# Optimization experiments

Hardware: AMD Instinct MI355X
Metric: run time of the kernel (lower is better)

The kernel has to match this reference:

```python
import jax, jax.numpy as jnp
import numpy as np

HEADS = 8
DIM_HEAD = 64
SCALE = DIM_HEAD ** -0.5

def _split_heads(x):
    # [B, N, H*D] -> [B, H, N, D]
    B, N, _ = x.shape
    return x.reshape(B, N, HEADS, DIM_HEAD).transpose(0, 2, 1, 3)

def _merge_heads(x):
    # [B, H, N, D] -> [B, N, H*D]
    B, H, N, D = x.shape
    return x.transpose(0, 2, 1, 3).reshape(B, N, H * D)

def setup_inputs() -> dict:
    key = jax.random.key(0)
    ks = jax.random.split(key, 6)
    B, N, DIM = 4, 2048, 512
    INNER = HEADS * DIM_HEAD
    return {
        "query1": jax.random.normal(ks[0], (B, N, DIM), dtype=jnp.float32),
        "query2": jax.random.normal(ks[1], (B, N, DIM), dtype=jnp.float32),
        "key_value": jax.random.normal(ks[2], (B, N, DIM), dtype=jnp.float32),
        "Wq1": jax.random.normal(ks[3], (DIM, INNER), dtype=jnp.float32) * (DIM ** -0.5),
        "Wq2": jax.random.normal(ks[4], (DIM, INNER), dtype=jnp.float32) * (DIM ** -0.5),
        "Wkv": jax.random.normal(ks[5], (DIM, 2 * INNER), dtype=jnp.float32) * (DIM ** -0.5),
    }

def reference(query1, query2, key_value, Wq1, Wq2, Wkv):
    q1 = _split_heads(query1 @ Wq1)          # [B,H,N,D]
    q2 = _split_heads(query2 @ Wq2)          # [B,H,N,D]
    kv = key_value @ Wkv                     # [B,N,2*inner]
    k_, v_ = jnp.split(kv, 2, axis=-1)
    k = _split_heads(k_)                     # [B,H,N,D]
    v = _split_heads(v_)                     # [B,H,N,D]
    dots1 = jnp.einsum('bhnd,bhmd->bhnm', q1, k) * SCALE
    dots2 = jnp.einsum('bhnd,bhmd->bhnm', q2, k) * SCALE
    attn1 = jax.nn.softmax(dots1, axis=-1)
    attn2 = jax.nn.softmax(dots2, axis=-1)
    out1 = _merge_heads(jnp.einsum('bhnm,bhmd->bhnd', attn1, v))
    out2 = _merge_heads(jnp.einsum('bhnm,bhmd->bhnd', attn2, v))
    return (out1, out2)
```

## Files before the change

kernel.cpp:

```cpp
#include <hip/hip_runtime.h>
#include <hip/hip_bf16.h>
#include <stdint.h>

typedef __attribute__((ext_vector_type(8))) short bf16x8;
typedef __attribute__((ext_vector_type(4))) float f32x4;
typedef __attribute__((ext_vector_type(4))) int int4v;
typedef __attribute__((ext_vector_type(2))) unsigned int uint2v;

#define MFMA16(a,b,c) __builtin_amdgcn_mfma_f32_16x16x32_bf16((a),(b),(c),0,0,0)

__device__ __forceinline__ unsigned short f2bf(float x) {
  unsigned u = __float_as_uint(x);
  u += 0x7FFFu + ((u >> 16) & 1u);
  return (unsigned short)(u >> 16);
}

__global__ __launch_bounds__(256) void convWT_kernel(
    const float* __restrict__ Wq1, const float* __restrict__ Wq2,
    const float* __restrict__ Wkv, unsigned short* __restrict__ WT) {
  __shared__ float tile[32][33];
  int ct = blockIdx.x & 63, kt = blockIdx.x >> 6;
  int tx = threadIdx.x & 31, ty = threadIdx.x >> 5;
  int c = ct * 32;
  const float* W; int c0; int ldw;
  if (c < 512)       { W = Wq1; c0 = c;        ldw = 512; }
  else if (c < 1024) { W = Wq2; c0 = c - 512;  ldw = 512; }
  else               { W = Wkv; c0 = c - 1024; ldw = 1024; }
#pragma unroll
  for (int rep = 0; rep < 4; ++rep) {
    int k = kt * 32 + ty + rep * 8;
    tile[ty + rep * 8][tx] = W[(size_t)k * ldw + c0 + tx];
  }
  __syncthreads();
#pragma unroll
  for (int rep = 0; rep < 4; ++rep) {
    int cl = ty + rep * 8;
    WT[(size_t)(c + cl) * 512 + kt * 32 + tx] = f2bf(tile[tx][cl]);
  }
}

__global__ __launch_bounds__(256) void gemm_kernel(
    const float* __restrict__ q1, const float* __restrict__ q2,
    const float* __restrict__ kv, const unsigned short* __restrict__ WT,
    unsigned short* __restrict__ C) {
  __shared__ unsigned short As[128 * 64];
  __shared__ unsigned short Bs[128 * 64];
  int bn = blockIdx.x & 15, bm = blockIdx.x >> 4;
  int seg = bn >> 2; if (seg > 2) seg = 2;
  const float* A = (seg == 0) ? q1 : (seg == 1) ? q2 : kv;
  int t = threadIdx.x;
  int l = t & 63, w = t >> 6;
  int i = l & 15, G = l >> 4;
  int wr = w >> 1, wc = w & 1;
  f32x4 acc[4][4];
#pragma unroll
  for (int m = 0; m < 4; ++m)
#pragma unroll
    for (int n = 0; n < 4; ++n) acc[m][n] = (f32x4){0.f, 0.f, 0.f, 0.f};

  for (int k0 = 0; k0 < 512; k0 += 64) {
    __syncthreads();
#pragma unroll
    for (int r2 = 0; r2 < 4; ++r2) {
      int idx = r2 * 256 + t;
      int row = idx >> 3, c8 = (idx & 7) * 8;
      const float* ab = A + (size_t)(bm * 128 + row) * 512 + k0 + c8;
      float4 fa = *(const float4*)ab;
      float4 fb = *(const float4*)(ab + 4);
      unsigned u0, u1, u2, u3;
      asm("v_cvt_pk_bf16_f32 %0, %1, %2" : "=v"(u0) : "v"(fa.x), "v"(fa.y));
      asm("v_cvt_pk_bf16_f32 %0, %1, %2" : "=v"(u1) : "v"(fa.z), "v"(fa.w));
      asm("v_cvt_pk_bf16_f32 %0, %1, %2" : "=v"(u2) : "v"(fb.x), "v"(fb.y));
      asm("v_cvt_pk_bf16_f32 %0, %1, %2" : "=v"(u3) : "v"(fb.z), "v"(fb.w));
      int4v av = {(int)u0, (int)u1, (int)u2, (int)u3};
      *(int4v*)(&As[row * 64 + c8]) = av;
      *(int4v*)(&Bs[row * 64 + c8]) =
          *(const int4v*)(WT + (size_t)(bn * 128 + row) * 512 + k0 + c8);
    }
    __syncthreads();
#pragma unroll
    for (int kk = 0; kk < 2; ++kk) {
      bf16x8 af[4], bfv[4];
#pragma unroll
      for (int m = 0; m < 4; ++m)
        af[m] = *(const bf16x8*)(&As[(wr * 64 + m * 16 + i) * 64 + kk * 32 + G * 8]);
#pragma unroll
      for (int n = 0; n < 4; ++n)
        bfv[n] = *(const bf16x8*)(&Bs[(wc * 64 + n * 16 + i) * 64 + kk * 32 + G * 8]);
#pragma unroll
      for (int m = 0; m < 4; ++m)
#pragma unroll
        for (int n = 0; n < 4; ++n)
          acc[m][n] = MFMA16(af[m], bfv[n], acc[m][n]);
    }
  }
  float sc = (bn < 8) ? 0.18033688011112042f : 1.0f;
#pragma unroll
  for (int m = 0; m < 4; ++m)
#pragma unroll
    for (int n = 0; n < 4; ++n)
#pragma unroll
      for (int r = 0; r < 4; ++r)
        C[(size_t)(bm * 128 + wr * 64 + m * 16 + G * 4 + r) * 2048 +
          bn * 128 + wc * 64 + n * 16 + i] = f2bf(acc[m][n][r] * sc);
}

__global__ __launch_bounds__(256) void vtT_kernel(
    const unsigned short* __restrict__ C, unsigned short* __restrict__ Vt) {
  __shared__ unsigned short tile[32][33];
  int idx = blockIdx.x;
  int nt = idx & 63, dt = (idx >> 6) & 1, bh = idx >> 7;
  int b = bh >> 3, h = bh & 7;
  int tx = threadIdx.x & 31, ty = threadIdx.x >> 5;
#pragma unroll
  for (int rep = 0; rep < 4; ++rep) {
    int n = nt * 32 + ty + rep * 8;
    tile[ty + rep * 8][tx] =
        C[(size_t)(b * 2048 + n) * 2048 + 1536 + h * 64 + dt * 32 + tx];
  }
  __syncthreads();
#pragma unroll
  for (int rep = 0; rep < 4; ++rep) {
    int dl = ty + rep * 8;
    Vt[((size_t)bh * 64 + dt * 32 + dl) * 2048 + nt * 32 + tx] = tile[tx][dl];
  }
}

__global__ __launch_bounds__(256, 2) void attn_kernel(
    const unsigned short* __restrict__ C, const unsigned short* __restrict__ Vt,
    float* __restrict__ out) {
  __shared__ unsigned short smem[8192];

  int hw = blockIdx.x;
  int virt = (hw & 7) * 128 + (hw >> 3);
  int qt = virt & 15, br = (virt >> 4) & 1, h = (virt >> 5) & 7, b = virt >> 8;

  int t = threadIdx.x;
  int l = t & 63, w = t >> 6;
  int i = l & 15, G = l >> 4;
  int qrow0 = qt * 128 + w * 32;

  const unsigned short* Qb = C + (size_t)(b * 2048 + qrow0) * 2048 + br * 512 + h * 64;
  float* Ob = out + (size_t)br * (4ull * 2048 * 512) +
              (size_t)(b * 2048 + qrow0) * 512 + h * 64;

  const unsigned short* gK = C + (size_t)(b * 2048 + w * 8 + (l >> 3)) * 2048 +
                             1024 + h * 64 + (l & 7) * 8;
  const unsigned short* gV = Vt + (size_t)(b * 8 + h) * 131072 +
                             (size_t)(w * 16 + (l >> 2)) * 2048 + (l & 3) * 8;
  int Koff = (w * 8 + (l >> 3)) * 64 + (((l & 7) ^ (l >> 3)) * 8);
  int Voff = 2048 + (w * 16 + (l >> 2)) * 32 + (l & 3) * 8;

  bf16x8 qf[2][2];
#pragma unroll
  for (int rt = 0; rt < 2; ++rt)
#pragma unroll
    for (int c = 0; c < 2; ++c)
      qf[rt][c] = *(const bf16x8*)(Qb + (size_t)(rt * 16 + i) * 2048 + c * 32 + G * 8);

  f32x4 o[2][4];
  float lsum[2];
#pragma unroll
  for (int rt = 0; rt < 2; ++rt) {
    lsum[rt] = 0.f;
#pragma unroll
    for (int dt = 0; dt < 4; ++dt) o[rt][dt] = (f32x4){0.f, 0.f, 0.f, 0.f};
  }

  auto compute = [&](const unsigned short* Kc) {
    const unsigned short* Vc = Kc + 2048;
    bf16x8 kf[2][2];
#pragma unroll
    for (int jt = 0; jt < 2; ++jt)
#pragma unroll
      for (int c = 0; c < 2; ++c)
        kf[jt][c] = *(const bf16x8*)(Kc + (jt * 16 + i) * 64 +
                                     (((c * 4 + G) ^ (i & 7)) * 8));
    f32x4 s[2][2];
#pragma unroll
    for (int jt = 0; jt < 2; ++jt)
#pragma unroll
      for (int rt = 0; rt < 2; ++rt) {
        s[jt][rt] = MFMA16(kf[jt][0], qf[rt][0], ((f32x4){0.f, 0.f, 0.f, 0.f}));
        s[jt][rt] = MFMA16(kf[jt][1], qf[rt][1], s[jt][rt]);
      }
    bf16x8 vf[4];
#pragma unroll
    for (int dt = 0; dt < 4; ++dt)
      vf[dt] = *(const bf16x8*)(Vc + (dt * 16 + i) * 32 + G * 8);

#pragma unroll
    for (int rt = 0; rt < 2; ++rt) {
      float p[8];
#pragma unroll
      for (int jt = 0; jt < 2; ++jt)
#pragma unroll
        for (int r = 0; r < 4; ++r)
          p[jt * 4 + r] = __builtin_amdgcn_exp2f(s[jt][rt][r]);
      lsum[rt] += ((p[0] + p[1]) + (p[2] + p[3])) + ((p[4] + p[5]) + (p[6] + p[7]));
      unsigned w0, w1, w2, w3;
      asm("v_cvt_pk_bf16_f32 %0, %1, %2" : "=v"(w0) : "v"(p[0]), "v"(p[1]));
      asm("v_cvt_pk_bf16_f32 %0, %1, %2" : "=v"(w1) : "v"(p[2]), "v"(p[3]));
      asm("v_cvt_pk_bf16_f32 %0, %1, %2" : "=v"(w2) : "v"(p[4]), "v"(p[5]));
      asm("v_cvt_pk_bf16_f32 %0, %1, %2" : "=v"(w3) : "v"(p[6]), "v"(p[7]));
      uint2v t02 = __builtin_amdgcn_permlane32_swap(w0, w2, false, false);
      uint2v n02 = __builtin_amdgcn_permlane16_swap(t02[0], t02[1], false, false);
      uint2v t13 = __builtin_amdgcn_permlane32_swap(w1, w3, false, false);
      uint2v n13 = __builtin_amdgcn_permlane16_swap(t13[0], t13[1], false, false);
      bf16x8 pf;
      ((unsigned*)&pf)[0] = n02[0]; ((unsigned*)&pf)[1] = n13[0];
      ((unsigned*)&pf)[2] = n02[1]; ((unsigned*)&pf)[3] = n13[1];
#pragma unroll
      for (int dt = 0; dt < 4; ++dt)
        o[rt][dt] = MFMA16(pf, vf[dt], o[rt][dt]);
    }
  };

  int4v rKa = *(const int4v*)gK;
  int4v rVa = *(const int4v*)gV;
  *(int4v*)(&smem[Koff]) = rKa;
  *(int4v*)(&smem[Voff]) = rVa;
  rKa = *(const int4v*)(gK + 2ull * 32 * 2048);
  rVa = *(const int4v*)(gV + 2 * 32);
  int4v rKb = *(const int4v*)(gK + 1ull * 32 * 2048);
  int4v rVb = *(const int4v*)(gV + 1 * 32);

  for (int kt2 = 0; kt2 < 32; ++kt2) {
    int kt = kt2 * 2;
    __syncthreads();
    *(int4v*)(&smem[4096 + Koff]) = rKb;
    *(int4v*)(&smem[4096 + Voff]) = rVb;
    {
      int n3 = (kt + 3 > 63) ? 63 : kt + 3;
      rKb = *(const int4v*)(gK + (size_t)n3 * 32 * 2048);
      rVb = *(const int4v*)(gV + n3 * 32);
    }
    compute(smem);
    __syncthreads();
    if (kt2 < 31) {
      *(int4v*)(&smem[Koff]) = rKa;
      *(int4v*)(&smem[Voff]) = rVa;
    }
    {
      int n4 = (kt + 4 > 63) ? 63 : kt + 4;
      rKa = *(const int4v*)(gK + (size_t)n4 * 32 * 2048);
      rVa = *(const int4v*)(gV + n4 * 32);
    }
    compute(smem + 4096);
  }

#pragma unroll
  for (int rt = 0; rt < 2; ++rt) {
    float ls = lsum[rt];
    ls += __shfl_xor(ls, 16);
    ls += __shfl_xor(ls, 32);
    f32x4 inv;
#pragma unroll
    for (int r = 0; r < 4; ++r) inv[r] = 1.0f / __shfl(ls, G * 4 + r);
#pragma unroll
    for (int dt = 0; dt < 4; ++dt)
#pragma unroll
      for (int r = 0; r < 4; ++r)
        Ob[(size_t)(rt * 16 + G * 4 + r) * 512 + dt * 16 + i] = o[rt][dt][r] * inv[r];
  }
}

extern "C" void kernel_launch(void* const* d_in, const int* in_sizes, int n_in,
                              void* d_out, int out_size, void* d_ws, size_t ws_size,
                              hipStream_t stream) {
  const float* q1  = (const float*)d_in[0];
  const float* q2  = (const float*)d_in[1];
  const float* kv  = (const float*)d_in[2];
  const float* Wq1 = (const float*)d_in[3];
  const float* Wq2 = (const float*)d_in[4];
  const float* Wkv = (const float*)d_in[5];
  float* out = (float*)d_out;
  char* ws = (char*)d_ws;
  unsigned short* WT = (unsigned short*)ws;
  unsigned short* Cb = (unsigned short*)(ws + 2097152);
  unsigned short* Vt = (unsigned short*)(ws + 35651584);

  convWT_kernel<<<1024, 256, 0, stream>>>(Wq1, Wq2, Wkv, WT);
  gemm_kernel<<<1024, 256, 0, stream>>>(q1, q2, kv, WT, Cb);
  vtT_kernel<<<4096, 256, 0, stream>>>(Cb, Vt);
  attn_kernel<<<1024, 256, 0, stream>>>(Cb, Vt, out);
}
```

Baseline: 135.1 us.

## Use 64-key tiles with one sync per step and MFMA row sums

The attention loop now stages 64 keys per step instead of 32, so each iteration does one __syncthreads over a double buffer that is twice as large. V tiles are stored with 64-element rows and an XOR swizzle to reduce LDS bank conflicts. The softmax denominator is accumulated by an extra MFMA against a ones vector, which removes the scalar exp adds and the final cross-lane shuffles. LDS use doubles to 32 KB per block, which could limit occupancy, and the row sums now come from bf16-rounded probabilities.

```diff
diff --git a/kernel.cpp b/kernel.cpp
--- a/kernel.cpp
+++ b/kernel.cpp
@@ -129,7 +129,7 @@
 __global__ __launch_bounds__(256, 2) void attn_kernel(
     const unsigned short* __restrict__ C, const unsigned short* __restrict__ Vt,
     float* __restrict__ out) {
-  __shared__ unsigned short smem[8192];
+  __shared__ unsigned short smem[16384];
 
   int hw = blockIdx.x;
   int virt = (hw & 7) * 128 + (hw >> 3);
@@ -148,8 +148,11 @@
                              1024 + h * 64 + (l & 7) * 8;
   const unsigned short* gV = Vt + (size_t)(b * 8 + h) * 131072 +
                              (size_t)(w * 16 + (l >> 2)) * 2048 + (l & 3) * 8;
-  int Koff = (w * 8 + (l >> 3)) * 64 + (((l & 7) ^ (l >> 3)) * 8);
-  int Voff = 2048 + (w * 16 + (l >> 2)) * 32 + (l & 3) * 8;
+  int Koff0 = (w * 8 + (l >> 3)) * 64 + (((l & 7) ^ (l >> 3)) * 8);
+  int Koff1 = Koff0 + 2048;
+  int vrow = w * 16 + (l >> 2);
+  int Voff0 = 4096 + vrow * 64 + ((((l & 3) + 0) ^ ((l >> 2) & 7)) * 8);
+  int Voff1 = 4096 + vrow * 64 + ((((l & 3) + 4) ^ ((l >> 2) & 7)) * 8);
 
   bf16x8 qf[2][2];
 #pragma unroll
@@ -159,104 +162,108 @@
       qf[rt][c] = *(const bf16x8*)(Qb + (size_t)(rt * 16 + i) * 2048 + c * 32 + G * 8);
 
   f32x4 o[2][4];
-  float lsum[2];
+  f32x4 lacc[2];
 #pragma unroll
   for (int rt = 0; rt < 2; ++rt) {
-    lsum[rt] = 0.f;
+    lacc[rt] = (f32x4){0.f, 0.f, 0.f, 0.f};
 #pragma unroll
     for (int dt = 0; dt < 4; ++dt) o[rt][dt] = (f32x4){0.f, 0.f, 0.f, 0.f};
   }
 
-  auto compute = [&](const unsigned short* Kc) {
-    const unsigned short* Vc = Kc + 2048;
-    bf16x8 kf[2][2];
-#pragma unroll
-    for (int jt = 0; jt < 2; ++jt)
-#pragma unroll
-      for (int c = 0; c < 2; ++c)
-        kf[jt][c] = *(const bf16x8*)(Kc + (jt * 16 + i) * 64 +
-                                     (((c * 4 + G) ^ (i & 7)) * 8));
-    f32x4 s[2][2];
-#pragma unroll
-    for (int jt = 0; jt < 2; ++jt)
+  const short ob = (short)0x3F80;
+  bf16x8 onesf = {ob, ob, ob, ob, ob, ob, ob, ob};
+
+  auto compute = [&](const unsigned short* buf) {
+#pragma unroll
+    for (int st = 0; st < 2; ++st) {
+      bf16x8 kf[2][2];
+#pragma unroll
+      for (int jt = 0; jt < 2; ++jt)
+#pragma unroll
+        for (int cc = 0; cc < 2; ++cc)
+          kf[jt][cc] = *(const bf16x8*)(buf + (st * 32 + jt * 16 + i) * 64 +
+                                        (((cc * 4 + G) ^ (i & 7)) * 8));
+      f32x4 s[2][2];
+#pragma unroll
+      for (int jt = 0; jt < 2; ++jt)
+#pragma unroll
+        for (int rt = 0; rt < 2; ++rt) {
+          s[jt][rt] = MFMA16(kf[jt][0], qf[rt][0], ((f32x4){0.f, 0.f, 0.f, 0.f}));
+          s[jt][rt] = MFMA16(kf[jt][1], qf[rt][1], s[jt][rt]);
+        }
+      bf16x8 vf[4];
+#pragma unroll
+      for (int dt = 0; dt < 4; ++dt)
+        vf[dt] = *(const bf16x8*)(buf + 4096 + (dt * 16 + i) * 64 +
+                                  (((st * 4 + G) ^ (i & 7)) * 8));
+
 #pragma unroll
       for (int rt = 0; rt < 2; ++rt) {
-        s[jt][rt] = MFMA16(kf[jt][0], qf[rt][0], ((f32x4){0.f, 0.f, 0.f, 0.f}));
-        s[jt][rt] = MFMA16(kf[jt][1], qf[rt][1], s[jt][rt]);
+        float p[8];
+#pragma unroll
+        for (int jt = 0; jt < 2; ++jt)
+#pragma unroll
+          for (int r = 0; r < 4; ++r)
+            p[jt * 4 + r] = __builtin_amdgcn_exp2f(s[jt][rt][r]);
+        unsigned w0, w1, w2, w3;
+        asm("v_cvt_pk_bf16_f32 %0, %1, %2" : "=v"(w0) : "v"(p[0]), "v"(p[1]));
+        asm("v_cvt_pk_bf16_f32 %0, %1, %2" : "=v"(w1) : "v"(p[2]), "v"(p[3]));
+        asm("v_cvt_pk_bf16_f32 %0, %1, %2" : "=v"(w2) : "v"(p[4]), "v"(p[5]));
+        asm("v_cvt_pk_bf16_f32 %0, %1, %2" : "=v"(w3) : "v"(p[6]), "v"(p[7]));
+        uint2v t02 = __builtin_amdgcn_permlane32_swap(w0, w2, false, false);
+        uint2v n02 = __builtin_amdgcn_permlane16_swap(t02[0], t02[1], false, false);
+        uint2v t13 = __builtin_amdgcn_permlane32_swap(w1, w3, false, false);
+        uint2v n13 = __builtin_amdgcn_permlane16_swap(t13[0], t13[1], false, false);
+        bf16x8 pf;
+        ((unsigned*)&pf)[0] = n02[0]; ((unsigned*)&pf)[1] = n13[0];
+        ((unsigned*)&pf)[2] = n02[1]; ((unsigned*)&pf)[3] = n13[1];
+        lacc[rt] = MFMA16(pf, onesf, lacc[rt]);
+#pragma unroll
+        for (int dt = 0; dt < 4; ++dt)
+          o[rt][dt] = MFMA16(pf, vf[dt], o[rt][dt]);
       }
-    bf16x8 vf[4];
-#pragma unroll
-    for (int dt = 0; dt < 4; ++dt)
-      vf[dt] = *(const bf16x8*)(Vc + (dt * 16 + i) * 32 + G * 8);
-
-#pragma unroll
-    for (int rt = 0; rt < 2; ++rt) {
-      float p[8];
-#pragma unroll
-      for (int jt = 0; jt < 2; ++jt)
-#pragma unroll
-        for (int r = 0; r < 4; ++r)
-          p[jt * 4 + r] = __builtin_amdgcn_exp2f(s[jt][rt][r]);
-      lsum[rt] += ((p[0] + p[1]) + (p[2] + p[3])) + ((p[4] + p[5]) + (p[6] + p[7]));
-      unsigned w0, w1, w2, w3;
-      asm("v_cvt_pk_bf16_f32 %0, %1, %2" : "=v"(w0) : "v"(p[0]), "v"(p[1]));
-      asm("v_cvt_pk_bf16_f32 %0, %1, %2" : "=v"(w1) : "v"(p[2]), "v"(p[3]));
-      asm("v_cvt_pk_bf16_f32 %0, %1, %2" : "=v"(w2) : "v"(p[4]), "v"(p[5]));
-      asm("v_cvt_pk_bf16_f32 %0, %1, %2" : "=v"(w3) : "v"(p[6]), "v"(p[7]));
-      uint2v t02 = __builtin_amdgcn_permlane32_swap(w0, w2, false, false);
-      uint2v n02 = __builtin_amdgcn_permlane16_swap(t02[0], t02[1], false, false);
-      uint2v t13 = __builtin_amdgcn_permlane32_swap(w1, w3, false, false);
-      uint2v n13 = __builtin_amdgcn_permlane16_swap(t13[0], t13[1], false, false);
-      bf16x8 pf;
-      ((unsigned*)&pf)[0] = n02[0]; ((unsigned*)&pf)[1] = n13[0];
-      ((unsigned*)&pf)[2] = n02[1]; ((unsigned*)&pf)[3] = n13[1];
-#pragma unroll
-      for (int dt = 0; dt < 4; ++dt)
-        o[rt][dt] = MFMA16(pf, vf[dt], o[rt][dt]);
     }
   };
 
-  int4v rKa = *(const int4v*)gK;
-  int4v rVa = *(const int4v*)gV;
-  *(int4v*)(&smem[Koff]) = rKa;
-  *(int4v*)(&smem[Voff]) = rVa;
-  rKa = *(const int4v*)(gK + 2ull * 32 * 2048);
-  rVa = *(const int4v*)(gV + 2 * 32);
-  int4v rKb = *(const int4v*)(gK + 1ull * 32 * 2048);
-  int4v rVb = *(const int4v*)(gV + 1 * 32);
-
-  for (int kt2 = 0; kt2 < 32; ++kt2) {
-    int kt = kt2 * 2;
+  int4v rK0 = *(const int4v*)gK;
+  int4v rK1 = *(const int4v*)(gK + 32ull * 2048);
+  int4v rV0 = *(const int4v*)gV;
+  int4v rV1 = *(const int4v*)(gV + 32);
+  *(int4v*)(&smem[Koff0]) = rK0;
+  *(int4v*)(&smem[Koff1]) = rK1;
+  *(int4v*)(&smem[Voff0]) = rV0;
+  *(int4v*)(&smem[Voff1]) = rV1;
+  rK0 = *(const int4v*)(gK + 64ull * 2048);
+  rK1 = *(const int4v*)(gK + 96ull * 2048);
+  rV0 = *(const int4v*)(gV + 64);
+  rV1 = *(const int4v*)(gV + 96);
+
+  unsigned short* cur = smem;
+  unsigned short* nxt = smem + 8192;
+  for (int T = 0; T < 32; ++T) {
     __syncthreads();
-    *(int4v*)(&smem[4096 + Koff]) = rKb;
-    *(int4v*)(&smem[4096 + Voff]) = rVb;
+    if (T < 31) {
+      *(int4v*)(&nxt[Koff0]) = rK0;
+      *(int4v*)(&nxt[Koff1]) = rK1;
+      *(int4v*)(&nxt[Voff0]) = rV0;
+      *(int4v*)(&nxt[Voff1]) = rV1;
+    }
     {
-      int n3 = (kt + 3 > 63) ? 63 : kt + 3;
-      rKb = *(const int4v*)(gK + (size_t)n3 * 32 * 2048);
-      rVb = *(const int4v*)(gV + n3 * 32);
-    }
-    compute(smem);
-    __syncthreads();
-    if (kt2 < 31) {
-      *(int4v*)(&smem[Koff]) = rKa;
-      *(int4v*)(&smem[Voff]) = rVa;
-    }
-    {
-      int n4 = (kt + 4 > 63) ? 63 : kt + 4;
-      rKa = *(const int4v*)(gK + (size_t)n4 * 32 * 2048);
-      rVa = *(const int4v*)(gV + n4 * 32);
-    }
-    compute(smem + 4096);
+      int Tn = (T + 2 > 31) ? 31 : T + 2;
+      rK0 = *(const int4v*)(gK + (size_t)Tn * 64 * 2048);
+      rK1 = *(const int4v*)(gK + (size_t)Tn * 64 * 2048 + 32ull * 2048);
+      rV0 = *(const int4v*)(gV + Tn * 64);
+      rV1 = *(const int4v*)(gV + Tn * 64 + 32);
+    }
+    compute(cur);
+    unsigned short* tmp = cur; cur = nxt; nxt = tmp;
   }
 
 #pragma unroll
   for (int rt = 0; rt < 2; ++rt) {
-    float ls = lsum[rt];
-    ls += __shfl_xor(ls, 16);
-    ls += __shfl_xor(ls, 32);
     f32x4 inv;
 #pragma unroll
-    for (int r = 0; r < 4; ++r) inv[r] = 1.0f / __shfl(ls, G * 4 + r);
+    for (int r = 0; r < 4; ++r) inv[r] = 1.0f / lacc[rt][r];
 #pragma unroll
     for (int dt = 0; dt < 4; ++dt)
 #pragma unroll
```

After: 134.5 us. Within noise of the previous version (-0.5%).
